# Performance work log

Hardware: AMD Instinct MI355X
Metric: run time of the kernel (lower is better)

## Reference

```python
import jax, jax.numpy as jnp
import numpy as np

ALPHA = 0.2   # LeakyReLU negative slope
BN_EPS = 1e-5
NEG_INF = -9e15  # same masking constant as the torch source


def make_quaternion_mul(kernel):
    # kernel: [in_features//4, out_features]; returns hamilton [in_features, out_features]
    r, i, j, k = jnp.split(kernel, 4, axis=1)
    r2 = jnp.concatenate([r, -i, -j, -k], axis=1)
    i2 = jnp.concatenate([i,  r, -k,  j], axis=1)
    j2 = jnp.concatenate([j,  k,  r, -i], axis=1)
    k2 = jnp.concatenate([k, -j,  i,  r], axis=1)
    return jnp.concatenate([r2, i2, j2, k2], axis=0)


def setup_inputs() -> dict:
    key = jax.random.key(0)
    k1, k2, k3, k4 = jax.random.split(key, 4)
    N, IN_F, OUT_F = 8192, 1024, 256
    inp = jax.random.normal(k1, (N, IN_F), dtype=jnp.float32)
    adj = jax.random.randint(k2, (N, N), 0, 2, dtype=jnp.int32)
    # xavier-uniform-like init scales
    W = jax.random.uniform(k3, (IN_F // 4, OUT_F), dtype=jnp.float32,
                           minval=-1.0, maxval=1.0) * np.sqrt(6.0 / (IN_F // 4 + OUT_F))
    a = jax.random.uniform(k4, (2 * OUT_F, 1), dtype=jnp.float32,
                           minval=-1.0, maxval=1.0) * np.sqrt(6.0 / (2 * OUT_F + 1))
    gamma = jnp.ones((OUT_F,), dtype=jnp.float32)
    beta = jnp.zeros((OUT_F,), dtype=jnp.float32)
    return {"input": inp, "adj": adj, "W": W, "a": a, "gamma": gamma, "beta": beta}


def reference(input, adj, W, a, gamma, beta):
    hamilton = make_quaternion_mul(W)            # [IN_F, OUT_F]
    h = input @ hamilton                         # [N, OUT_F]
    F_out = h.shape[1]
    # e[i, j] = leakyrelu(concat(h_i, h_j) . a) = leakyrelu(h_i.a1 + h_j.a2)
    a1 = a[:F_out, 0]
    a2 = a[F_out:, 0]
    e = jax.nn.leaky_relu((h @ a1)[:, None] + (h @ a2)[None, :],
                          negative_slope=ALPHA)  # [N, N]
    e = jnp.where(adj > 0, e, NEG_INF)
    attention = jax.nn.softmax(e, axis=1)        # masked softmax over neighbors
    h_prime = attention @ h                      # [N, OUT_F]
    # BatchNorm1d (training mode: batch statistics, biased variance)
    mean = jnp.mean(h_prime, axis=0)
    var = jnp.var(h_prime, axis=0)
    h_norm = (h_prime - mean) * jax.lax.rsqrt(var + BN_EPS) * gamma + beta
    return jax.nn.elu(h_norm)                    # concat=True -> elu
```

## Files before the change

kernel.cpp:

```cpp
#include <hip/hip_runtime.h>
#include <stdint.h>

#define ALPHA 0.2f
#define LOG2E 1.4426950408889634f

typedef __attribute__((ext_vector_type(8))) short short8;
typedef __attribute__((ext_vector_type(4))) float f32x4;
typedef __attribute__((ext_vector_type(16))) float f32x16;
typedef __attribute__((ext_vector_type(4))) int int4v;
typedef __attribute__((ext_vector_type(2))) unsigned int uint2v;

#if __has_builtin(__builtin_amdgcn_exp2f)
#define EXP2(x) __builtin_amdgcn_exp2f(x)
#else
#define EXP2(x) exp2f(x)
#endif

__device__ __forceinline__ unsigned short f2bf(float x){
  union { float f; uint32_t u; } v; v.f = x;
  uint32_t u = v.u;
  u += 0x7FFFu + ((u >> 16) & 1u);
  return (unsigned short)(u >> 16);
}
__device__ __forceinline__ float bf2f(unsigned short s){
  union { uint32_t u; float f; } v; v.u = ((uint32_t)s) << 16; return v.f;
}
__device__ __forceinline__ unsigned cvt_pk_bf16(float lo, float hi){
  unsigned r;
  asm("v_cvt_pk_bf16_f32 %0, %1, %2" : "=v"(r) : "v"(lo), "v"(hi));
  return r;
}
__device__ __forceinline__ unsigned encf(float x){
  unsigned u = __float_as_uint(x);
  return (u & 0x80000000u) ? ~u : (u | 0x80000000u);
}
__device__ __forceinline__ float decf(unsigned u){
  return (u & 0x80000000u) ? __uint_as_float(u & 0x7FFFFFFFu) : __uint_as_float(~u);
}

__global__ void k_ham(const float* __restrict__ W, unsigned short* __restrict__ hi,
                      unsigned short* __restrict__ lo, unsigned* __restrict__ S2enc,
                      float* __restrict__ gsum, float* __restrict__ gsumsq){
  if (blockIdx.x == 0){
    if (threadIdx.x == 0) S2enc[0] = 0u;
    gsum[threadIdx.x] = 0.f; gsumsq[threadIdx.x] = 0.f;
  }
  int id = blockIdx.x * 256 + threadIdx.x;
  int c = id >> 10, k = id & 1023;
  int b = k >> 8, r = k & 255;
  int cb = c >> 6, col = c & 63;
  const int   comp[4][4] = {{0,1,2,3},{1,0,3,2},{2,3,0,1},{3,2,1,0}};
  const float sgn [4][4] = {{1.f,-1.f,-1.f,-1.f},{1.f,1.f,-1.f,1.f},
                            {1.f,1.f,1.f,-1.f},{1.f,-1.f,1.f,1.f}};
  float v = sgn[b][cb] * W[r * 256 + comp[b][cb] * 64 + col];
  unsigned short h = f2bf(v);
  hi[id] = h;
  lo[id] = f2bf(v - bf2f(h));
}

__global__ __launch_bounds__(256) void k_work(
    const float* __restrict__ inp, const int* __restrict__ adj,
    const unsigned short* __restrict__ hamHi, const unsigned short* __restrict__ hamLo,
    const float* __restrict__ avec, unsigned short* __restrict__ hTt,
    float* __restrict__ s1s, float* __restrict__ s2s, unsigned* __restrict__ S2enc,
    unsigned long long* __restrict__ bm){
  if (blockIdx.x >= 256){
    const int lane = threadIdx.x & 63;
    const size_t wid = ((size_t)(blockIdx.x - 256) * 256 + threadIdx.x) >> 6;
    const size_t W0 = wid * 1024;
    unsigned long long b[16];
#pragma unroll
    for (int q = 0; q < 4; ++q){
      int4v a = *(const int4v*)(adj + W0 + 256*q + 4*lane);
#pragma unroll
      for (int k = 0; k < 4; ++k) b[4*q + k] = __ballot(a[k] > 0);
    }
    if (lane < 16){
      unsigned long long v = b[0];
#pragma unroll
      for (int m = 1; m < 16; ++m) v = (lane == m) ? b[m] : v;
      bm[W0/64 + lane] = v;
    }
    return;
  }
  int i0 = blockIdx.x * 32;
  int w = threadIdx.x >> 6, lane = threadIdx.x & 63;
  int mi = lane & 15, g = lane >> 4;
  int cbase = w * 64;
  f32x4 acc[2][4];
#pragma unroll
  for (int mf=0; mf<2; ++mf)
#pragma unroll
    for (int nf=0; nf<4; ++nf) acc[mf][nf] = (f32x4){0.f,0.f,0.f,0.f};

  for (int k0 = 0; k0 < 1024; k0 += 32){
    short8 ah[2], al[2];
#pragma unroll
    for (int mf=0; mf<2; ++mf){
      const float* ap = inp + (size_t)(i0 + 16*mf + mi) * 1024 + k0 + 8*g;
      f32x4 x0 = *(const f32x4*)ap;
      f32x4 x1 = *(const f32x4*)(ap + 4);
#pragma unroll
      for (int e=0; e<8; ++e){
        float x = (e < 4) ? x0[e] : x1[e-4];
        unsigned short h = f2bf(x);
        ah[mf][e] = (short)h;
        al[mf][e] = (short)f2bf(x - bf2f(h));
      }
    }
    short8 bh[4], bl[4];
#pragma unroll
    for (int nf=0; nf<4; ++nf){
      size_t off = (size_t)(cbase + 16*nf + mi) * 1024 + k0 + 8*g;
      bh[nf] = *(const short8*)(hamHi + off);
      bl[nf] = *(const short8*)(hamLo + off);
    }
#pragma unroll
    for (int mf=0; mf<2; ++mf)
#pragma unroll
      for (int nf=0; nf<4; ++nf){
        acc[mf][nf] = __builtin_amdgcn_mfma_f32_16x16x32_bf16(ah[mf], bh[nf], acc[mf][nf], 0,0,0);
        acc[mf][nf] = __builtin_amdgcn_mfma_f32_16x16x32_bf16(ah[mf], bl[nf], acc[mf][nf], 0,0,0);
        acc[mf][nf] = __builtin_amdgcn_mfma_f32_16x16x32_bf16(al[mf], bh[nf], acc[mf][nf], 0,0,0);
      }
  }
  float p1[2][4] = {{0,0,0,0},{0,0,0,0}}, p2[2][4] = {{0,0,0,0},{0,0,0,0}};
#pragma unroll
  for (int nf=0; nf<4; ++nf){
    int c = cbase + 16*nf + mi;
    float a1c = avec[c], a2c = avec[256 + c];
#pragma unroll
    for (int mf=0; mf<2; ++mf){
      int jg = (i0 + 16*mf + 4*g) >> 3;
      uint2v u;
      u[0] = (uint32_t)f2bf(acc[mf][nf][0]) | ((uint32_t)f2bf(acc[mf][nf][1]) << 16);
      u[1] = (uint32_t)f2bf(acc[mf][nf][2]) | ((uint32_t)f2bf(acc[mf][nf][3]) << 16);
      *(uint2v*)(hTt + (size_t)jg * 2048 + c * 8 + (g & 1) * 4) = u;
#pragma unroll
      for (int rg=0; rg<4; ++rg){
        p1[mf][rg] += acc[mf][nf][rg] * a1c;
        p2[mf][rg] += acc[mf][nf][rg] * a2c;
      }
    }
  }
#pragma unroll
  for (int off=1; off<16; off<<=1){
#pragma unroll
    for (int mf=0; mf<2; ++mf)
#pragma unroll
      for (int rg=0; rg<4; ++rg){
        p1[mf][rg] += __shfl_xor(p1[mf][rg], off);
        p2[mf][rg] += __shfl_xor(p2[mf][rg], off);
      }
  }
  __shared__ float red1[4][32], red2[4][32];
  if (mi == 0){
#pragma unroll
    for (int mf=0; mf<2; ++mf)
#pragma unroll
      for (int rg=0; rg<4; ++rg){
        red1[w][16*mf + 4*g + rg] = p1[mf][rg];
        red2[w][16*mf + 4*g + rg] = p2[mf][rg];
      }
  }
  __syncthreads();
  if (threadIdx.x < 32){
    int r = threadIdx.x;
    float v1 = red1[0][r] + red1[1][r] + red1[2][r] + red1[3][r];
    float v2 = red2[0][r] + red2[1][r] + red2[2][r] + red2[3][r];
    s1s[i0 + r] = v1 * LOG2E;
    float v2s = v2 * LOG2E;
    s2s[i0 + r] = v2s;
    float m = v2s;
#pragma unroll
    for (int off=1; off<32; off<<=1) m = fmaxf(m, __shfl_xor(m, off));
    if (r == 0) atomicMax(S2enc, encf(m));
  }
}

#define STAGE(t, b) do { \
    const unsigned short* sp_ = hTt + (size_t)jw0 * 256 + (size_t)(t) * 16384; \
    _Pragma("unroll") \
    for (int r_ = 0; r_ < 8; ++r_){ \
      int ch_ = tid + r_*256; \
      __builtin_amdgcn_global_load_lds((const __attribute__((address_space(1))) void*)(const void*)(sp_ + ch_*8), \
          (__attribute__((address_space(3))) void*)(void*)&hbuf[(b)][ch_*8], 16, 0, 0); \
    } } while(0)

__global__ __launch_bounds__(256,2) void k_attn(
    const unsigned long long* __restrict__ bm, const unsigned short* __restrict__ hTt,
    const float* __restrict__ s1s, const float* __restrict__ s2s,
    const unsigned* __restrict__ S2enc, float* __restrict__ accp, float* __restrict__ Zp){
  __shared__ unsigned short hbuf[2][256*64];
  __shared__ float s2l[1024];
  const int tid = threadIdx.x;
  const int id = blockIdx.x;
  const int js = id & 7;
  const int rb = id >> 3;
  const int w = tid >> 6, lane = tid & 63;
  const int r31 = lane & 31, hi = lane >> 5;
  const int i0w = rb * 128 + w * 32;
  const int jw0 = js * 1024;

  { f32x4 v = *(const f32x4*)(s2s + jw0 + tid*4); *(f32x4*)&s2l[tid*4] = v; }

  const float S2MAX = decf(S2enc[0]);
  const float s1v = s1s[i0w + r31];
  const float xm = s1v + S2MAX;
  const float m2 = fmaxf(xm, ALPHA * xm);
  const float P1 = s1v - m2;
  const float P2 = ALPHA * s1v - m2;

  const unsigned long long* brow = bm + (size_t)(i0w + r31) * 128 + js * 16;

  f32x16 acc[8];
#pragma unroll
  for (int nf=0; nf<8; ++nf)
#pragma unroll
    for (int q=0; q<16; ++q) acc[nf][q] = 0.f;
  float zac = 0.f;

  unsigned long long Wc[4], Wn[4];
#pragma unroll
  for (int k=0;k<4;++k) Wc[k] = brow[k];
  STAGE(0, 0);
  __syncthreads();

  for (int tile = 0; tile < 16; ++tile){
    const int buf = tile & 1;
    if ((tile & 3) == 0){
      if (tile){
#pragma unroll
        for (int k=0;k<4;++k) Wc[k] = Wn[k];
      }
      if (tile + 4 < 16){
        const unsigned long long* p = brow + (tile >> 2)*4 + 4;
#pragma unroll
        for (int k=0;k<4;++k) Wn[k] = p[k];
      }
    }
    if (tile < 15) STAGE(tile + 1, buf ^ 1);
#pragma unroll
    for (int ks=0; ks<4; ++ks){
      f32x4 sa = *(const f32x4*)&s2l[tile*64 + ks*16 + hi*8];
      f32x4 sb = *(const f32x4*)&s2l[tile*64 + ks*16 + hi*8 + 4];
      const int sh0 = ((tile & 3) << 4) + (ks << 2) + (hi << 1);
      unsigned tt[4];
#pragma unroll
      for (int k=0;k<4;++k) tt[k] = (unsigned)(Wc[k] >> sh0);
      float pe[8];
#pragma unroll
      for (int e=0; e<8; ++e){
        float s2e = (e < 4) ? sa[e] : sb[e-4];
        float t1 = P1 + s2e;
        float t2 = fmaf(ALPHA, s2e, P2);
        float p = EXP2(fmaxf(t1, t2));
        p = ((tt[e & 3] >> (e >> 2)) & 1u) ? p : 0.f;
        zac += p;
        pe[e] = p;
      }
      union { short8 s; unsigned u[4]; } pa;
#pragma unroll
      for (int wd=0; wd<4; ++wd) pa.u[wd] = cvt_pk_bf16(pe[2*wd], pe[2*wd+1]);
      const int jbase = (2*ks + hi) * 2048;
#pragma unroll
      for (int nf=0; nf<8; ++nf){
        short8 b = *(const short8*)&hbuf[buf][jbase + (32*nf + r31)*8];
        acc[nf] = __builtin_amdgcn_mfma_f32_32x32x16_bf16(pa.s, b, acc[nf], 0,0,0);
      }
    }
    __syncthreads();
  }
  zac += __shfl_xor(zac, 32);
  if (lane < 32) Zp[js*8192 + i0w + lane] = zac;
#pragma unroll
  for (int nf=0; nf<8; ++nf){
    const int c = 32*nf + r31;
#pragma unroll
    for (int reg=0; reg<16; ++reg){
      const int roff = (reg&3) + 8*(reg>>2) + 4*hi;
      accp[(size_t)(js*8192 + i0w + roff)*256 + c] = acc[nf][reg];
    }
  }
}

__global__ void k_stats(const float* __restrict__ accp, const float* __restrict__ Zp,
                        float* __restrict__ hp, float* __restrict__ gsum,
                        float* __restrict__ gsumsq){
  int c = threadIdx.x;
  int r0 = blockIdx.x * 32;
  float s = 0.f, sq = 0.f;
  for (int r=0; r<32; ++r){
    int i = r0 + r;
    float z = 0.f;
#pragma unroll
    for (int s8=0; s8<8; ++s8) z += Zp[s8*8192 + i];
    float inv = (z > 0.f) ? 1.f / z : 0.f;
    size_t o = (size_t)i * 256 + c;
    float v = 0.f;
#pragma unroll
    for (int s8=0; s8<8; ++s8) v += accp[o + (size_t)s8*8192*256];
    v *= inv;
    hp[o] = v;
    s += v; sq += v*v;
  }
  atomicAdd(&gsum[c], s);
  atomicAdd(&gsumsq[c], sq);
}

__global__ void k_bnelu(float* __restrict__ out, const float* __restrict__ gsum,
                        const float* __restrict__ gsumsq, const float* __restrict__ gamma,
                        const float* __restrict__ beta){
  int id = blockIdx.x * 256 + threadIdx.x;
  int c = id & 255;
  float mean = gsum[c] * (1.f/8192.f);
  float var  = gsumsq[c] * (1.f/8192.f) - mean*mean;
  float x = (out[id] - mean) * rsqrtf(var + 1e-5f) * gamma[c] + beta[c];
  out[id] = x > 0.f ? x : (EXP2(x * LOG2E) - 1.f);
}

extern "C" void kernel_launch(void* const* d_in, const int* in_sizes, int n_in,
                              void* d_out, int out_size, void* d_ws, size_t ws_size,
                              hipStream_t stream){
  const float* inp   = (const float*)d_in[0];
  const int*   adj   = (const int*)d_in[1];
  const float* W     = (const float*)d_in[2];
  const float* avec  = (const float*)d_in[3];
  const float* gamma = (const float*)d_in[4];
  const float* beta  = (const float*)d_in[5];
  float* out = (float*)d_out;

  char* ws = (char*)d_ws;
  float* accp = (float*)ws;
  float* Zp   = accp + (size_t)8*8192*256;
  unsigned short* hamHi = (unsigned short*)(Zp + 65536);
  unsigned short* hamLo = hamHi + 262144;
  unsigned short* hTt   = hamLo + 262144;
  float* s1s = (float*)(hTt + 2097152);
  float* s2s = s1s + 8192;
  unsigned* S2enc = (unsigned*)(s2s + 8192);
  float* gsum   = (float*)(S2enc + 64);
  float* gsumsq = gsum + 256;
  unsigned long long* bm = (unsigned long long*)(gsumsq + 256);

  k_ham<<<1024, 256, 0, stream>>>(W, hamHi, hamLo, S2enc, gsum, gsumsq);
  k_work<<<16640, 256, 0, stream>>>(inp, adj, hamHi, hamLo, avec, hTt, s1s, s2s, S2enc, bm);
  k_attn<<<512, 256, 0, stream>>>(bm, hTt, s1s, s2s, S2enc, accp, Zp);
  k_stats<<<256, 256, 0, stream>>>(accp, Zp, out, gsum, gsumsq);
  k_bnelu<<<8192, 256, 0, stream>>>(out, gsum, gsumsq, gamma, beta);
}
```

Baseline: 168.0 us.

## Load attention B operands directly from global, drop LDS staging; widen stats grid

The attention kernel no longer stages h tiles into double-buffered LDS with async global-to-LDS loads and per-tile barriers. Each lane now reads its MFMA B fragments straight from global memory (relying on L2 and cache reuse across the four waves) and issues the eight MFMAs back to back. This removes LDS traffic and block synchronisation, at the cost of redundant global/L2 reads and more exposed load latency. Separately, the stats kernel runs more blocks over fewer rows each, giving more parallelism at the price of more atomics.

After: 210.0 us. 25.0% more time.

```diff
diff --git a/kernel.cpp b/kernel.cpp
--- a/kernel.cpp
+++ b/kernel.cpp
@@ -178,20 +178,10 @@
   }
 }
 
-#define STAGE(t, b) do { \
-    const unsigned short* sp_ = hTt + (size_t)jw0 * 256 + (size_t)(t) * 16384; \
-    _Pragma("unroll") \
-    for (int r_ = 0; r_ < 8; ++r_){ \
-      int ch_ = tid + r_*256; \
-      __builtin_amdgcn_global_load_lds((const __attribute__((address_space(1))) void*)(const void*)(sp_ + ch_*8), \
-          (__attribute__((address_space(3))) void*)(void*)&hbuf[(b)][ch_*8], 16, 0, 0); \
-    } } while(0)
-
 __global__ __launch_bounds__(256,2) void k_attn(
     const unsigned long long* __restrict__ bm, const unsigned short* __restrict__ hTt,
     const float* __restrict__ s1s, const float* __restrict__ s2s,
     const unsigned* __restrict__ S2enc, float* __restrict__ accp, float* __restrict__ Zp){
-  __shared__ unsigned short hbuf[2][256*64];
   __shared__ float s2l[1024];
   const int tid = threadIdx.x;
   const int id = blockIdx.x;
@@ -203,6 +193,7 @@
   const int jw0 = js * 1024;
 
   { f32x4 v = *(const f32x4*)(s2s + jw0 + tid*4); *(f32x4*)&s2l[tid*4] = v; }
+  __syncthreads();
 
   const float S2MAX = decf(S2enc[0]);
   const float s1v = s1s[i0w + r31];
@@ -212,6 +203,7 @@
   const float P2 = ALPHA * s1v - m2;
 
   const unsigned long long* brow = bm + (size_t)(i0w + r31) * 128 + js * 16;
+  const unsigned short* hbase = hTt + ((size_t)(jw0 >> 3) + hi) * 2048 + r31 * 8;
 
   f32x16 acc[8];
 #pragma unroll
@@ -223,11 +215,8 @@
   unsigned long long Wc[4], Wn[4];
 #pragma unroll
   for (int k=0;k<4;++k) Wc[k] = brow[k];
-  STAGE(0, 0);
-  __syncthreads();
 
   for (int tile = 0; tile < 16; ++tile){
-    const int buf = tile & 1;
     if ((tile & 3) == 0){
       if (tile){
 #pragma unroll
@@ -239,9 +228,17 @@
         for (int k=0;k<4;++k) Wn[k] = p[k];
       }
     }
-    if (tile < 15) STAGE(tile + 1, buf ^ 1);
 #pragma unroll
     for (int ks=0; ks<4; ++ks){
+      const unsigned short* hp_ = hbase + (size_t)(tile*8 + ks*2) * 2048;
+      short8 b0 = *(const short8*)(hp_);
+      short8 b1 = *(const short8*)(hp_ + 256);
+      short8 b2 = *(const short8*)(hp_ + 512);
+      short8 b3 = *(const short8*)(hp_ + 768);
+      short8 b4 = *(const short8*)(hp_ + 1024);
+      short8 b5 = *(const short8*)(hp_ + 1280);
+      short8 b6 = *(const short8*)(hp_ + 1536);
+      short8 b7 = *(const short8*)(hp_ + 1792);
       f32x4 sa = *(const f32x4*)&s2l[tile*64 + ks*16 + hi*8];
       f32x4 sb = *(const f32x4*)&s2l[tile*64 + ks*16 + hi*8 + 4];
       const int sh0 = ((tile & 3) << 4) + (ks << 2) + (hi << 1);
@@ -262,14 +259,15 @@
       union { short8 s; unsigned u[4]; } pa;
 #pragma unroll
       for (int wd=0; wd<4; ++wd) pa.u[wd] = cvt_pk_bf16(pe[2*wd], pe[2*wd+1]);
-      const int jbase = (2*ks + hi) * 2048;
-#pragma unroll
-      for (int nf=0; nf<8; ++nf){
-        short8 b = *(const short8*)&hbuf[buf][jbase + (32*nf + r31)*8];
-        acc[nf] = __builtin_amdgcn_mfma_f32_32x32x16_bf16(pa.s, b, acc[nf], 0,0,0);
-      }
-    }
-    __syncthreads();
+      acc[0] = __builtin_amdgcn_mfma_f32_32x32x16_bf16(pa.s, b0, acc[0], 0,0,0);
+      acc[1] = __builtin_amdgcn_mfma_f32_32x32x16_bf16(pa.s, b1, acc[1], 0,0,0);
+      acc[2] = __builtin_amdgcn_mfma_f32_32x32x16_bf16(pa.s, b2, acc[2], 0,0,0);
+      acc[3] = __builtin_amdgcn_mfma_f32_32x32x16_bf16(pa.s, b3, acc[3], 0,0,0);
+      acc[4] = __builtin_amdgcn_mfma_f32_32x32x16_bf16(pa.s, b4, acc[4], 0,0,0);
+      acc[5] = __builtin_amdgcn_mfma_f32_32x32x16_bf16(pa.s, b5, acc[5], 0,0,0);
+      acc[6] = __builtin_amdgcn_mfma_f32_32x32x16_bf16(pa.s, b6, acc[6], 0,0,0);
+      acc[7] = __builtin_amdgcn_mfma_f32_32x32x16_bf16(pa.s, b7, acc[7], 0,0,0);
+    }
   }
   zac += __shfl_xor(zac, 32);
   if (lane < 32) Zp[js*8192 + i0w + lane] = zac;
@@ -288,9 +286,9 @@
                         float* __restrict__ hp, float* __restrict__ gsum,
                         float* __restrict__ gsumsq){
   int c = threadIdx.x;
-  int r0 = blockIdx.x * 32;
+  int r0 = blockIdx.x * 8;
   float s = 0.f, sq = 0.f;
-  for (int r=0; r<32; ++r){
+  for (int r=0; r<8; ++r){
     int i = r0 + r;
     float z = 0.f;
 #pragma unroll
@@ -346,6 +344,6 @@
   k_ham<<<1024, 256, 0, stream>>>(W, hamHi, hamLo, S2enc, gsum, gsumsq);
   k_work<<<16640, 256, 0, stream>>>(inp, adj, hamHi, hamLo, avec, hTt, s1s, s2s, S2enc, bm);
   k_attn<<<512, 256, 0, stream>>>(bm, hTt, s1s, s2s, S2enc, accp, Zp);
-  k_stats<<<256, 256, 0, stream>>>(accp, Zp, out, gsum, gsumsq);
+  k_stats<<<1024, 256, 0, stream>>>(accp, Zp, out, gsum, gsumsq);
   k_bnelu<<<8192, 256, 0, stream>>>(out, gsum, gsumsq, gamma, beta);
 }
```

## Triple-buffer attention tiles with vmcnt waits and widen stats grid

Applied to the files above, without the earlier changes.

The attention kernel now streams smaller 32-row h tiles through a three-slot LDS ring, prefetching two tiles ahead. Each iteration uses a partial s_waitcnt vmcnt plus one raw barrier instead of a full __syncthreads after compute, so global-to-LDS loads overlap the MFMA work for longer. The stats kernel is also launched with four times as many blocks, each handling 8 rows, to expose more parallelism. The cost is more atomics per column, and the hand-written wait counts depend on how the compiler orders memory operations.

After: 183.0 us. 8.9% more time.

```diff
diff --git a/kernel.cpp b/kernel.cpp
--- a/kernel.cpp
+++ b/kernel.cpp
@@ -178,10 +178,10 @@
   }
 }
 
-#define STAGE(t, b) do { \
-    const unsigned short* sp_ = hTt + (size_t)jw0 * 256 + (size_t)(t) * 16384; \
+#define STAGE3(t, b) do { \
+    const unsigned short* sp_ = hTt + (size_t)(jw0 >> 3) * 2048 + (size_t)(t) * 8192; \
     _Pragma("unroll") \
-    for (int r_ = 0; r_ < 8; ++r_){ \
+    for (int r_ = 0; r_ < 4; ++r_){ \
       int ch_ = tid + r_*256; \
       __builtin_amdgcn_global_load_lds((const __attribute__((address_space(1))) void*)(const void*)(sp_ + ch_*8), \
           (__attribute__((address_space(3))) void*)(void*)&hbuf[(b)][ch_*8], 16, 0, 0); \
@@ -191,7 +191,7 @@
     const unsigned long long* __restrict__ bm, const unsigned short* __restrict__ hTt,
     const float* __restrict__ s1s, const float* __restrict__ s2s,
     const unsigned* __restrict__ S2enc, float* __restrict__ accp, float* __restrict__ Zp){
-  __shared__ unsigned short hbuf[2][256*64];
+  __shared__ unsigned short hbuf[3][8192];
   __shared__ float s2l[1024];
   const int tid = threadIdx.x;
   const int id = blockIdx.x;
@@ -223,28 +223,37 @@
   unsigned long long Wc[4], Wn[4];
 #pragma unroll
   for (int k=0;k<4;++k) Wc[k] = brow[k];
-  STAGE(0, 0);
-  __syncthreads();
-
-  for (int tile = 0; tile < 16; ++tile){
-    const int buf = tile & 1;
-    if ((tile & 3) == 0){
+
+  STAGE3(0, 0);
+  STAGE3(1, 1);
+
+  int bcur = 0;
+  for (int tile = 0; tile < 32; ++tile){
+    if (tile < 31) asm volatile("s_waitcnt vmcnt(4) lgkmcnt(0)" ::: "memory");
+    else           asm volatile("s_waitcnt vmcnt(0) lgkmcnt(0)" ::: "memory");
+    __builtin_amdgcn_sched_barrier(0);
+    __builtin_amdgcn_s_barrier();
+    if ((tile & 7) == 0){
       if (tile){
 #pragma unroll
         for (int k=0;k<4;++k) Wc[k] = Wn[k];
       }
-      if (tile + 4 < 16){
-        const unsigned long long* p = brow + (tile >> 2)*4 + 4;
+      if (tile + 8 < 32){
+        const unsigned long long* p = brow + (tile >> 3)*4 + 4;
 #pragma unroll
         for (int k=0;k<4;++k) Wn[k] = p[k];
       }
     }
-    if (tile < 15) STAGE(tile + 1, buf ^ 1);
-#pragma unroll
-    for (int ks=0; ks<4; ++ks){
-      f32x4 sa = *(const f32x4*)&s2l[tile*64 + ks*16 + hi*8];
-      f32x4 sb = *(const f32x4*)&s2l[tile*64 + ks*16 + hi*8 + 4];
-      const int sh0 = ((tile & 3) << 4) + (ks << 2) + (hi << 1);
+    if (tile < 30){
+      int bst = bcur + 2; if (bst >= 3) bst -= 3;
+      STAGE3(tile + 2, bst);
+    }
+#pragma unroll
+    for (int ks=0; ks<2; ++ks){
+      const int jj = tile*2 + ks;
+      f32x4 sa = *(const f32x4*)&s2l[jj*16 + hi*8];
+      f32x4 sb = *(const f32x4*)&s2l[jj*16 + hi*8 + 4];
+      const int sh0 = ((jj & 15) << 2) + (hi << 1);
       unsigned tt[4];
 #pragma unroll
       for (int k=0;k<4;++k) tt[k] = (unsigned)(Wc[k] >> sh0);
@@ -265,12 +274,13 @@
       const int jbase = (2*ks + hi) * 2048;
 #pragma unroll
       for (int nf=0; nf<8; ++nf){
-        short8 b = *(const short8*)&hbuf[buf][jbase + (32*nf + r31)*8];
+        short8 b = *(const short8*)&hbuf[bcur][jbase + (32*nf + r31)*8];
         acc[nf] = __builtin_amdgcn_mfma_f32_32x32x16_bf16(pa.s, b, acc[nf], 0,0,0);
       }
     }
-    __syncthreads();
-  }
+    bcur = bcur + 1; if (bcur >= 3) bcur = 0;
+  }
+
   zac += __shfl_xor(zac, 32);
   if (lane < 32) Zp[js*8192 + i0w + lane] = zac;
 #pragma unroll
@@ -288,9 +298,9 @@
                         float* __restrict__ hp, float* __restrict__ gsum,
                         float* __restrict__ gsumsq){
   int c = threadIdx.x;
-  int r0 = blockIdx.x * 32;
+  int r0 = blockIdx.x * 8;
   float s = 0.f, sq = 0.f;
-  for (int r=0; r<32; ++r){
+  for (int r=0; r<8; ++r){
     int i = r0 + r;
     float z = 0.f;
 #pragma unroll
@@ -346,6 +356,6 @@
   k_ham<<<1024, 256, 0, stream>>>(W, hamHi, hamLo, S2enc, gsum, gsumsq);
   k_work<<<16640, 256, 0, stream>>>(inp, adj, hamHi, hamLo, avec, hTt, s1s, s2s, S2enc, bm);
   k_attn<<<512, 256, 0, stream>>>(bm, hTt, s1s, s2s, S2enc, accp, Zp);
-  k_stats<<<256, 256, 0, stream>>>(accp, Zp, out, gsum, gsumsq);
+  k_stats<<<1024, 256, 0, stream>>>(accp, Zp, out, gsum, gsumsq);
   k_bnelu<<<8192, 256, 0, stream>>>(out, gsum, gsumsq, gamma, beta);
 }
```

## Split attention j-range inside 512-thread blocks, halving partial buffers and stats work

Applied to the files above, without the earlier changes.

The attention kernel now runs 512-thread blocks in which two wave groups each handle half of a 2048-column j-slice. Their accumulators are combined through LDS before writing, so only four j-split partials go to global memory instead of eight. This cuts the partial-sum write and read traffic in k_attn and k_stats, and k_stats is relaunched with more, smaller blocks. The Hamilton build kernel is also rewritten to transpose through LDS for coalesced writes. The cost is an extra LDS reduction and one block per CU with higher LDS use.

New measurement: 175.5 us. +4.5%, slower.

```diff
diff --git a/kernel.cpp b/kernel.cpp
--- a/kernel.cpp
+++ b/kernel.cpp
@@ -38,24 +38,42 @@
   return (u & 0x80000000u) ? __uint_as_float(u & 0x7FFFFFFFu) : __uint_as_float(~u);
 }
 
-__global__ void k_ham(const float* __restrict__ W, unsigned short* __restrict__ hi,
-                      unsigned short* __restrict__ lo, unsigned* __restrict__ S2enc,
-                      float* __restrict__ gsum, float* __restrict__ gsumsq){
+__global__ __launch_bounds__(256) void k_ham(
+    const float* __restrict__ W, unsigned short* __restrict__ hi,
+    unsigned short* __restrict__ lo, unsigned* __restrict__ S2enc,
+    float* __restrict__ gsum, float* __restrict__ gsumsq){
   if (blockIdx.x == 0){
     if (threadIdx.x == 0) S2enc[0] = 0u;
     gsum[threadIdx.x] = 0.f; gsumsq[threadIdx.x] = 0.f;
   }
-  int id = blockIdx.x * 256 + threadIdx.x;
-  int c = id >> 10, k = id & 1023;
-  int b = k >> 8, r = k & 255;
-  int cb = c >> 6, col = c & 63;
+  __shared__ float wlds[64 * 65];
+  const int t = threadIdx.x;
+  const int pair = blockIdx.x >> 2, rc = blockIdx.x & 3;
+  const int b = pair >> 2, cb = pair & 3;
   const int   comp[4][4] = {{0,1,2,3},{1,0,3,2},{2,3,0,1},{3,2,1,0}};
   const float sgn [4][4] = {{1.f,-1.f,-1.f,-1.f},{1.f,1.f,-1.f,1.f},
                             {1.f,1.f,1.f,-1.f},{1.f,-1.f,1.f,1.f}};
-  float v = sgn[b][cb] * W[r * 256 + comp[b][cb] * 64 + col];
-  unsigned short h = f2bf(v);
-  hi[id] = h;
-  lo[id] = f2bf(v - bf2f(h));
+  const int q = comp[b][cb];
+  const float s = sgn[b][cb];
+#pragma unroll
+  for (int rep = 0; rep < 16; ++rep){
+    int idx = rep * 256 + t;
+    int row = idx >> 6, col = idx & 63;
+    wlds[row * 65 + col] = W[(size_t)(rc*64 + row) * 256 + q*64 + col];
+  }
+  __syncthreads();
+#pragma unroll
+  for (int rep = 0; rep < 16; ++rep){
+    int idx = rep * 256 + t;
+    int col = idx >> 6, row = idx & 63;
+    float v = s * wlds[row * 65 + col];
+    int c = cb*64 + col;
+    int k = b*256 + rc*64 + row;
+    unsigned short h = f2bf(v);
+    size_t o = (size_t)c * 1024 + k;
+    hi[o] = h;
+    lo[o] = f2bf(v - bf2f(h));
+  }
 }
 
 __global__ __launch_bounds__(256) void k_work(
@@ -179,30 +197,32 @@
 }
 
 #define STAGE(t, b) do { \
-    const unsigned short* sp_ = hTt + (size_t)jw0 * 256 + (size_t)(t) * 16384; \
+    const unsigned short* sp_ = hTt + (size_t)(js*256 + hgrp*128 + (t)*8) * 2048; \
     _Pragma("unroll") \
     for (int r_ = 0; r_ < 8; ++r_){ \
-      int ch_ = tid + r_*256; \
+      int ch_ = htid + r_*256; \
       __builtin_amdgcn_global_load_lds((const __attribute__((address_space(1))) void*)(const void*)(sp_ + ch_*8), \
-          (__attribute__((address_space(3))) void*)(void*)&hbuf[(b)][ch_*8], 16, 0, 0); \
+          (__attribute__((address_space(3))) void*)(void*)&hbuf[hgrp][(b)][ch_*8], 16, 0, 0); \
     } } while(0)
 
-__global__ __launch_bounds__(256,2) void k_attn(
+__global__ __launch_bounds__(512,1) void k_attn(
     const unsigned long long* __restrict__ bm, const unsigned short* __restrict__ hTt,
     const float* __restrict__ s1s, const float* __restrict__ s2s,
     const unsigned* __restrict__ S2enc, float* __restrict__ accp, float* __restrict__ Zp){
-  __shared__ unsigned short hbuf[2][256*64];
-  __shared__ float s2l[1024];
+  __shared__ unsigned short hbuf[2][2][16384];
+  __shared__ float s2l[2048];
+  __shared__ float zbuf[128];
   const int tid = threadIdx.x;
   const int id = blockIdx.x;
-  const int js = id & 7;
-  const int rb = id >> 3;
+  const int js = (id & 7) >> 1;
+  const int rb = ((id >> 3) << 1) | (id & 1);
   const int w = tid >> 6, lane = tid & 63;
+  const int jhalf = w >> 2, rowg = w & 3;
   const int r31 = lane & 31, hi = lane >> 5;
-  const int i0w = rb * 128 + w * 32;
-  const int jw0 = js * 1024;
-
-  { f32x4 v = *(const f32x4*)(s2s + jw0 + tid*4); *(f32x4*)&s2l[tid*4] = v; }
+  const int i0w = rb * 128 + rowg * 32;
+  const int htid = tid & 255, hgrp = tid >> 8;
+
+  { f32x4 v = *(const f32x4*)(s2s + js*2048 + tid*4); *(f32x4*)&s2l[tid*4] = v; }
 
   const float S2MAX = decf(S2enc[0]);
   const float s1v = s1s[i0w + r31];
@@ -211,7 +231,7 @@
   const float P1 = s1v - m2;
   const float P2 = ALPHA * s1v - m2;
 
-  const unsigned long long* brow = bm + (size_t)(i0w + r31) * 128 + js * 16;
+  const unsigned long long* brow = bm + (size_t)(i0w + r31) * 128 + js * 32 + jhalf * 16;
 
   f32x16 acc[8];
 #pragma unroll
@@ -241,45 +261,63 @@
     }
     if (tile < 15) STAGE(tile + 1, buf ^ 1);
 #pragma unroll
-    for (int ks=0; ks<4; ++ks){
-      f32x4 sa = *(const f32x4*)&s2l[tile*64 + ks*16 + hi*8];
-      f32x4 sb = *(const f32x4*)&s2l[tile*64 + ks*16 + hi*8 + 4];
-      const int sh0 = ((tile & 3) << 4) + (ks << 2) + (hi << 1);
-      unsigned tt[4];
-#pragma unroll
-      for (int k=0;k<4;++k) tt[k] = (unsigned)(Wc[k] >> sh0);
-      float pe[8];
-#pragma unroll
-      for (int e=0; e<8; ++e){
-        float s2e = (e < 4) ? sa[e] : sb[e-4];
-        float t1 = P1 + s2e;
-        float t2 = fmaf(ALPHA, s2e, P2);
-        float p = EXP2(fmaxf(t1, t2));
-        p = ((tt[e & 3] >> (e >> 2)) & 1u) ? p : 0.f;
-        zac += p;
-        pe[e] = p;
-      }
-      union { short8 s; unsigned u[4]; } pa;
-#pragma unroll
-      for (int wd=0; wd<4; ++wd) pa.u[wd] = cvt_pk_bf16(pe[2*wd], pe[2*wd+1]);
-      const int jbase = (2*ks + hi) * 2048;
-#pragma unroll
-      for (int nf=0; nf<8; ++nf){
-        short8 b = *(const short8*)&hbuf[buf][jbase + (32*nf + r31)*8];
-        acc[nf] = __builtin_amdgcn_mfma_f32_32x32x16_bf16(pa.s, b, acc[nf], 0,0,0);
+    for (int ks=0; ks<2; ++ks){
+      const int so = jhalf*1024 + tile*64 + ks*32;
+#pragma unroll
+      for (int kt=0; kt<2; ++kt){
+        const int jj16 = 2*ks + kt;
+        f32x4 sa = *(const f32x4*)&s2l[jhalf*1024 + tile*64 + jj16*16 + hi*8];
+        f32x4 sb = *(const f32x4*)&s2l[jhalf*1024 + tile*64 + jj16*16 + hi*8 + 4];
+        const int sh0 = ((tile & 3) << 4) + (jj16 << 2) + (hi << 1);
+        unsigned tt[4];
+#pragma unroll
+        for (int k=0;k<4;++k) tt[k] = (unsigned)(Wc[k] >> sh0);
+        float pe[8];
+#pragma unroll
+        for (int e=0; e<8; ++e){
+          float s2e = (e < 4) ? sa[e] : sb[e-4];
+          float t1 = P1 + s2e;
+          float t2 = fmaf(ALPHA, s2e, P2);
+          float p = EXP2(fmaxf(t1, t2));
+          p = ((tt[e & 3] >> (e >> 2)) & 1u) ? p : 0.f;
+          zac += p;
+          pe[e] = p;
+        }
+        union { short8 s; unsigned u[4]; } pa;
+#pragma unroll
+        for (int wd=0; wd<4; ++wd) pa.u[wd] = cvt_pk_bf16(pe[2*wd], pe[2*wd+1]);
+        const int jbase = (2*jj16 + hi) * 2048;
+#pragma unroll
+        for (int nf=0; nf<8; ++nf){
+          short8 b = *(const short8*)&hbuf[jhalf][buf][jbase + (32*nf + r31)*8];
+          acc[nf] = __builtin_amdgcn_mfma_f32_32x32x16_bf16(pa.s, b, acc[nf], 0,0,0);
+        }
       }
     }
     __syncthreads();
   }
   zac += __shfl_xor(zac, 32);
-  if (lane < 32) Zp[js*8192 + i0w + lane] = zac;
-#pragma unroll
-  for (int nf=0; nf<8; ++nf){
-    const int c = 32*nf + r31;
-#pragma unroll
-    for (int reg=0; reg<16; ++reg){
-      const int roff = (reg&3) + 8*(reg>>2) + 4*hi;
-      accp[(size_t)(js*8192 + i0w + roff)*256 + c] = acc[nf][reg];
+  float* cmb = (float*)(void*)hbuf;
+  if (hgrp == 1){
+#pragma unroll
+    for (int nf=0; nf<8; ++nf)
+#pragma unroll
+      for (int reg=0; reg<16; ++reg)
+        cmb[(nf*16 + reg)*256 + htid] = acc[nf][reg];
+    if (lane < 32) zbuf[rowg*32 + lane] = zac;
+  }
+  __syncthreads();
+  if (hgrp == 0){
+    if (lane < 32) Zp[js*8192 + i0w + lane] = zac + zbuf[rowg*32 + lane];
+#pragma unroll
+    for (int nf=0; nf<8; ++nf){
+      const int c = 32*nf + r31;
+#pragma unroll
+      for (int reg=0; reg<16; ++reg){
+        const int roff = (reg&3) + 8*(reg>>2) + 4*hi;
+        accp[(size_t)(js*8192 + i0w + roff)*256 + c] =
+            acc[nf][reg] + cmb[(nf*16 + reg)*256 + htid];
+      }
     }
   }
 }
@@ -288,19 +326,15 @@
                         float* __restrict__ hp, float* __restrict__ gsum,
                         float* __restrict__ gsumsq){
   int c = threadIdx.x;
-  int r0 = blockIdx.x * 32;
+  int r0 = blockIdx.x * 8;
   float s = 0.f, sq = 0.f;
-  for (int r=0; r<32; ++r){
+  for (int r=0; r<8; ++r){
     int i = r0 + r;
-    float z = 0.f;
-#pragma unroll
-    for (int s8=0; s8<8; ++s8) z += Zp[s8*8192 + i];
+    float z = Zp[i] + Zp[8192 + i] + Zp[16384 + i] + Zp[24576 + i];
     float inv = (z > 0.f) ? 1.f / z : 0.f;
     size_t o = (size_t)i * 256 + c;
-    float v = 0.f;
-#pragma unroll
-    for (int s8=0; s8<8; ++s8) v += accp[o + (size_t)s8*8192*256];
-    v *= inv;
+    float v = (accp[o] + accp[o + (size_t)8192*256] + accp[o + (size_t)2*8192*256]
+               + accp[o + (size_t)3*8192*256]) * inv;
     hp[o] = v;
     s += v; sq += v*v;
   }
@@ -332,8 +366,8 @@
 
   char* ws = (char*)d_ws;
   float* accp = (float*)ws;
-  float* Zp   = accp + (size_t)8*8192*256;
-  unsigned short* hamHi = (unsigned short*)(Zp + 65536);
+  float* Zp   = accp + (size_t)4*8192*256;
+  unsigned short* hamHi = (unsigned short*)(Zp + 32768);
   unsigned short* hamLo = hamHi + 262144;
   unsigned short* hTt   = hamLo + 262144;
   float* s1s = (float*)(hTt + 2097152);
@@ -343,9 +377,9 @@
   float* gsumsq = gsum + 256;
   unsigned long long* bm = (unsigned long long*)(gsumsq + 256);
 
-  k_ham<<<1024, 256, 0, stream>>>(W, hamHi, hamLo, S2enc, gsum, gsumsq);
+  k_ham<<<64, 256, 0, stream>>>(W, hamHi, hamLo, S2enc, gsum, gsumsq);
   k_work<<<16640, 256, 0, stream>>>(inp, adj, hamHi, hamLo, avec, hTt, s1s, s2s, S2enc, bm);
-  k_attn<<<512, 256, 0, stream>>>(bm, hTt, s1s, s2s, S2enc, accp, Zp);
-  k_stats<<<256, 256, 0, stream>>>(accp, Zp, out, gsum, gsumsq);
+  k_attn<<<256, 512, 0, stream>>>(bm, hTt, s1s, s2s, S2enc, accp, Zp);
+  k_stats<<<1024, 256, 0, stream>>>(accp, Zp, out, gsum, gsumsq);
   k_bnelu<<<8192, 256, 0, stream>>>(out, gsum, gsumsq, gamma, beta);
 }
```
